# Kernel tuning notes

Measured on AMD Instinct MI355X. Metric: run time of the kernel, lower is better.

Reference implementation:

```python
import jax, jax.numpy as jnp
import numpy as np

NUM_HEADS = 16
LN_EPS = 1e-5


def setup_inputs() -> dict:
    key = jax.random.key(0)
    ks = jax.random.split(key, 5)
    B, S, H = 32768, 3, 1024
    scale = 1.0 / np.sqrt(H)
    return {
        "slots": jax.random.normal(ks[0], (B, S, H), dtype=jnp.float32),
        "in_proj_w": jax.random.normal(ks[1], (3 * H, H), dtype=jnp.float32) * scale,
        "in_proj_b": jax.random.normal(ks[2], (3 * H,), dtype=jnp.float32) * 0.02,
        "out_w": jax.random.normal(ks[3], (H, H), dtype=jnp.float32) * scale,
        "out_b": jax.random.normal(ks[4], (H,), dtype=jnp.float32) * 0.02,
        "ln_g": jnp.ones((H,), dtype=jnp.float32),
        "ln_b": jnp.zeros((H,), dtype=jnp.float32),
    }


def reference(slots, in_proj_w, in_proj_b, out_w, out_b, ln_g, ln_b):
    # slots: [B, 3, H]. Matches torch nn.MultiheadAttention (batch_first) in eval
    # mode (dropout inactive) followed by residual add + LayerNorm.
    B, S, H = slots.shape
    nh = NUM_HEADS
    dh = H // nh

    # fused QKV projection: torch does x @ in_proj_w.T + in_proj_b
    qkv = jnp.einsum("bsh,eh->bse", slots, in_proj_w) + in_proj_b  # [B,S,3H]
    q, k, v = jnp.split(qkv, 3, axis=-1)

    def heads(t):  # [B,S,H] -> [B,nh,S,dh]
        return t.reshape(B, S, nh, dh).transpose(0, 2, 1, 3)

    q, k, v = heads(q), heads(k), heads(v)

    scores = jnp.einsum("bnqd,bnkd->bnqk", q, k) / jnp.sqrt(jnp.asarray(dh, slots.dtype))
    attn = jax.nn.softmax(scores, axis=-1)  # [B,nh,3,3]
    ctx = jnp.einsum("bnqk,bnkd->bnqd", attn, v)  # [B,nh,3,dh]
    ctx = ctx.transpose(0, 2, 1, 3).reshape(B, S, H)

    attn_out = jnp.einsum("bsh,oh->bso", ctx, out_w) + out_b  # out_proj

    # residual + LayerNorm (dropout is identity at inference)
    y = slots + attn_out
    mu = jnp.mean(y, axis=-1, keepdims=True)
    var = jnp.mean(jnp.square(y - mu), axis=-1, keepdims=True)
    return (y - mu) / jnp.sqrt(var + LN_EPS) * ln_g + ln_b
```

## Files before the change

kernel.cpp:

```cpp
#include <hip/hip_runtime.h>
#include <stdint.h>

typedef unsigned short u16;
typedef float f32x4 __attribute__((ext_vector_type(4)));
typedef short bf16x8 __attribute__((ext_vector_type(8)));

__device__ __forceinline__ u16 f2bu(float f) {
  uint32_t x = __builtin_bit_cast(uint32_t, f);
  x += 0x7fffu + ((x >> 16) & 1u);
  return (u16)(x >> 16);
}
__device__ __forceinline__ float b2f(u16 u) {
  return __builtin_bit_cast(float, (uint32_t)u << 16);
}
__device__ __forceinline__ void gll16(const void* g, void* l) {
  __builtin_amdgcn_global_load_lds(
      (const __attribute__((address_space(1))) void*)g,
      (__attribute__((address_space(3))) void*)l, 16, 0, 0);
}

__global__ __launch_bounds__(256) void cvt_f32_bf16_kernel(
    const float* __restrict__ in, u16* __restrict__ out, int n4) {
  int i = blockIdx.x * 256 + threadIdx.x;
  const int stride = gridDim.x * 256;
  for (; i < n4; i += stride) {
    float4 f = reinterpret_cast<const float4*>(in)[i];
    ushort4 o;
    o.x = f2bu(f.x); o.y = f2bu(f.y); o.z = f2bu(f.z); o.w = f2bu(f.w);
    reinterpret_cast<ushort4*>(out)[i] = o;
  }
}

__global__ __launch_bounds__(512, 2) void gemm256_bt_bias(
    const u16* __restrict__ A, const u16* __restrict__ Bw,
    const float* __restrict__ bias, u16* __restrict__ C,
    int N, int K, int ntn) {
  __shared__ u16 lds[4][2][8192];
  const int tid = threadIdx.x;
  const int lane = tid & 63, wid = tid >> 6;
  const int wr = wid >> 2, wc = wid & 3;
  const int fr = lane & 15, kg = lane >> 4;

  const int cpx = (int)gridDim.x >> 3;
  const int bid = blockIdx.x;
  const int sid = (bid & 7) * cpx + (bid >> 3);
  const int mt = sid / ntn, nt = sid % ntn;

  const int srow = tid >> 2;
  const int scol = (tid & 3) ^ ((tid >> 3) & 3);
  const u16* Ag = A + (size_t)(mt * 256 + srow) * K + scol * 8;
  const u16* Bg = Bw + (size_t)(nt * 256 + srow) * K + scol * 8;
  const size_t rstep = (size_t)128 * K;

  const int sw = (fr >> 1) & 3;
  const int aoff = (wr * 128 + fr) * 32 + (kg ^ sw) * 8;
  const int boff = (wc * 64 + fr) * 32 + (kg ^ sw) * 8;

  f32x4 acc[8][4];
#pragma unroll
  for (int i = 0; i < 8; i++)
#pragma unroll
    for (int j = 0; j < 4; j++) acc[i][j] = f32x4{0.f, 0.f, 0.f, 0.f};

  const int NT = K >> 5;

#define STAGE(b, kt) do {                                   \
    const u16* a_ = Ag + (size_t)(kt) * 32;                 \
    const u16* b_ = Bg + (size_t)(kt) * 32;                 \
    gll16(a_,         &lds[(b)][0][wid * 512]);             \
    gll16(a_ + rstep, &lds[(b)][0][4096 + wid * 512]);      \
    gll16(b_,         &lds[(b)][1][wid * 512]);             \
    gll16(b_ + rstep, &lds[(b)][1][4096 + wid * 512]);      \
  } while (0)

  STAGE(0, 0);
  STAGE(1, 1);
  STAGE(2, 2);

  for (int t = 0; t < NT; t++) {
    if (t < NT - 2)       asm volatile("s_waitcnt vmcnt(8)" ::: "memory");
    else if (t == NT - 2) asm volatile("s_waitcnt vmcnt(4)" ::: "memory");
    else                  asm volatile("s_waitcnt vmcnt(0)" ::: "memory");
    __builtin_amdgcn_s_barrier();
    if (t + 3 < NT) STAGE((t + 3) & 3, t + 3);
    const u16* As = &lds[t & 3][0][0];
    const u16* Bs = &lds[t & 3][1][0];
    bf16x8 af[8], bfv[4];
#pragma unroll
    for (int mi = 0; mi < 8; mi++)
      af[mi] = *(const bf16x8*)&As[aoff + mi * 512];
#pragma unroll
    for (int nj = 0; nj < 4; nj++)
      bfv[nj] = *(const bf16x8*)&Bs[boff + nj * 512];
    __builtin_amdgcn_s_setprio(1);
#pragma unroll
    for (int mi = 0; mi < 8; mi++)
#pragma unroll
      for (int nj = 0; nj < 4; nj++)
        acc[mi][nj] = __builtin_amdgcn_mfma_f32_16x16x32_bf16(
            af[mi], bfv[nj], acc[mi][nj], 0, 0, 0);
    __builtin_amdgcn_s_setprio(0);
    asm volatile("s_waitcnt lgkmcnt(0)" ::: "memory");
    __builtin_amdgcn_sched_barrier(0);
  }
#undef STAGE

  const int crow0 = mt * 256 + wr * 128 + kg * 4;
  const int ccol0 = nt * 256 + wc * 64 + fr;
#pragma unroll
  for (int nj = 0; nj < 4; nj++) {
    const int col = ccol0 + nj * 16;
    const float bb = bias[col];
#pragma unroll
    for (int mi = 0; mi < 8; mi++) {
      const int r0 = crow0 + mi * 16;
      f32x4 v = acc[mi][nj];
#pragma unroll
      for (int r = 0; r < 4; r++)
        C[(size_t)(r0 + r) * N + col] = f2bu(v[r] + bb);
    }
  }
}

__global__ __launch_bounds__(256) void attn3_kernel(
    const u16* __restrict__ qkv, u16* __restrict__ ctx) {
  const int tid = threadIdx.x;
  const int lane = tid & 63, wid = tid >> 6;
  const int unit = blockIdx.x * 4 + wid;
  const int b = unit >> 2, hg = unit & 3;
  const size_t qbase = (size_t)b * 3 * 3072 + hg * 256 + lane * 4;

  float q[3][4], k[3][4], v[3][4];
#pragma unroll
  for (int s = 0; s < 3; s++) {
    ushort4 uq = *(const ushort4*)(qkv + qbase + (size_t)s * 3072);
    ushort4 uk = *(const ushort4*)(qkv + qbase + (size_t)s * 3072 + 1024);
    ushort4 uv = *(const ushort4*)(qkv + qbase + (size_t)s * 3072 + 2048);
    q[s][0] = b2f(uq.x); q[s][1] = b2f(uq.y); q[s][2] = b2f(uq.z); q[s][3] = b2f(uq.w);
    k[s][0] = b2f(uk.x); k[s][1] = b2f(uk.y); k[s][2] = b2f(uk.z); k[s][3] = b2f(uk.w);
    v[s][0] = b2f(uv.x); v[s][1] = b2f(uv.y); v[s][2] = b2f(uv.z); v[s][3] = b2f(uv.w);
  }

  float sc[3][3];
#pragma unroll
  for (int i = 0; i < 3; i++)
#pragma unroll
    for (int j = 0; j < 3; j++) {
      float p = q[i][0] * k[j][0] + q[i][1] * k[j][1] +
                q[i][2] * k[j][2] + q[i][3] * k[j][3];
      p += __shfl_xor(p, 1);
      p += __shfl_xor(p, 2);
      p += __shfl_xor(p, 4);
      p += __shfl_xor(p, 8);
      sc[i][j] = p;
    }

  float o[3][4];
#pragma unroll
  for (int i = 0; i < 3; i++) {
    float mx = fmaxf(sc[i][0], fmaxf(sc[i][1], sc[i][2]));
    float e0 = __expf((sc[i][0] - mx) * 0.125f);
    float e1 = __expf((sc[i][1] - mx) * 0.125f);
    float e2 = __expf((sc[i][2] - mx) * 0.125f);
    float inv = 1.f / (e0 + e1 + e2);
    e0 *= inv; e1 *= inv; e2 *= inv;
#pragma unroll
    for (int d = 0; d < 4; d++)
      o[i][d] = e0 * v[0][d] + e1 * v[1][d] + e2 * v[2][d];
  }

  const size_t obase = (size_t)b * 3 * 1024 + hg * 256 + lane * 4;
#pragma unroll
  for (int i = 0; i < 3; i++) {
    ushort4 ov;
    ov.x = f2bu(o[i][0]); ov.y = f2bu(o[i][1]);
    ov.z = f2bu(o[i][2]); ov.w = f2bu(o[i][3]);
    *(ushort4*)(ctx + obase + (size_t)i * 1024) = ov;
  }
}

__global__ __launch_bounds__(256) void ln_kernel(
    const float* __restrict__ slots, const u16* __restrict__ ao,
    const float* __restrict__ g, const float* __restrict__ bvec,
    float* __restrict__ out) {
  const int tid = threadIdx.x;
  const int lane = tid & 63, wid = tid >> 6;
  const int row = blockIdx.x * 4 + wid;
  const size_t rb = (size_t)row * 1024;

  float y[16];
  float sum = 0.f, sq = 0.f;
#pragma unroll
  for (int c = 0; c < 4; c++) {
    const int col = c * 256 + lane * 4;
    float4 sl = *(const float4*)(slots + rb + col);
    ushort4 a4 = *(const ushort4*)(ao + rb + col);
    float y0 = sl.x + b2f(a4.x), y1 = sl.y + b2f(a4.y);
    float y2 = sl.z + b2f(a4.z), y3 = sl.w + b2f(a4.w);
    y[c * 4 + 0] = y0; y[c * 4 + 1] = y1; y[c * 4 + 2] = y2; y[c * 4 + 3] = y3;
    sum += y0 + y1 + y2 + y3;
    sq += y0 * y0 + y1 * y1 + y2 * y2 + y3 * y3;
  }
#pragma unroll
  for (int m = 1; m < 64; m <<= 1) {
    sum += __shfl_xor(sum, m);
    sq  += __shfl_xor(sq, m);
  }
  const float mu = sum * (1.0f / 1024.0f);
  const float var = sq * (1.0f / 1024.0f) - mu * mu;
  const float rs = rsqrtf(var + 1e-5f);
#pragma unroll
  for (int c = 0; c < 4; c++) {
    const int col = c * 256 + lane * 4;
    float4 gg = *(const float4*)(g + col);
    float4 bb = *(const float4*)(bvec + col);
    float4 ov;
    ov.x = (y[c * 4 + 0] - mu) * rs * gg.x + bb.x;
    ov.y = (y[c * 4 + 1] - mu) * rs * gg.y + bb.y;
    ov.z = (y[c * 4 + 2] - mu) * rs * gg.z + bb.z;
    ov.w = (y[c * 4 + 3] - mu) * rs * gg.w + bb.w;
    *(float4*)(out + rb + col) = ov;
  }
}

extern "C" void kernel_launch(void* const* d_in, const int* in_sizes, int n_in,
                              void* d_out, int out_size, void* d_ws, size_t ws_size,
                              hipStream_t stream) {
  const float* slots = (const float*)d_in[0];
  const float* in_w  = (const float*)d_in[1];
  const float* in_b  = (const float*)d_in[2];
  const float* out_w = (const float*)d_in[3];
  const float* out_b = (const float*)d_in[4];
  const float* ln_g  = (const float*)d_in[5];
  const float* ln_b  = (const float*)d_in[6];
  float* out = (float*)d_out;

  const int M = 32768 * 3;

  char* ws = (char*)d_ws;
  u16* Abf   = (u16*)ws;
  u16* Winb  = (u16*)(ws + 201326592);
  u16* Woutb = (u16*)(ws + 207618048);
  u16* qkv   = (u16*)(ws + 209715200);

  cvt_f32_bf16_kernel<<<2048, 256, 0, stream>>>(slots, Abf, M * 1024 / 4);
  cvt_f32_bf16_kernel<<<2048, 256, 0, stream>>>(in_w, Winb, 3072 * 1024 / 4);
  cvt_f32_bf16_kernel<<<1024, 256, 0, stream>>>(out_w, Woutb, 1024 * 1024 / 4);

  gemm256_bt_bias<<<384 * 12, 512, 0, stream>>>(Abf, Winb, in_b, qkv, 3072, 1024, 12);

  attn3_kernel<<<32768, 256, 0, stream>>>(qkv, Abf);

  gemm256_bt_bias<<<384 * 4, 512, 0, stream>>>(Abf, Woutb, out_b, qkv, 1024, 1024, 4);

  ln_kernel<<<M / 4, 256, 0, stream>>>(slots, qkv, ln_g, ln_b, out);
}
```

Before: 1.374 ms.

## Split GEMM main loop into two half-phases interleaving LDS reads, staging, and MFMA

Restructures the bf16 GEMM K-loop into two phases per tile. Each phase loads half of the A fragments, issues half of the global-to-LDS staging (A or B) for a future tile, then runs half of the MFMAs, with barriers between phases. The goal is to overlap LDS reads and global loads with matrix math and to cut register pressure from holding all fragments at once. In exchange it adds barriers per iteration and more delicate vmcnt bookkeeping.

```diff
diff --git a/kernel.cpp b/kernel.cpp
--- a/kernel.cpp
+++ b/kernel.cpp
@@ -18,6 +18,7 @@
       (const __attribute__((address_space(1))) void*)g,
       (__attribute__((address_space(3))) void*)l, 16, 0, 0);
 }
+#define MEMFENCE asm volatile("" ::: "memory")
 
 __global__ __launch_bounds__(256) void cvt_f32_bf16_kernel(
     const float* __restrict__ in, u16* __restrict__ out, int n4) {
@@ -64,46 +65,74 @@
 
   const int NT = K >> 5;
 
-#define STAGE(b, kt) do {                                   \
+#define STAGE_A(b, kt) do {                                 \
     const u16* a_ = Ag + (size_t)(kt) * 32;                 \
-    const u16* b_ = Bg + (size_t)(kt) * 32;                 \
     gll16(a_,         &lds[(b)][0][wid * 512]);             \
     gll16(a_ + rstep, &lds[(b)][0][4096 + wid * 512]);      \
+  } while (0)
+#define STAGE_B(b, kt) do {                                 \
+    const u16* b_ = Bg + (size_t)(kt) * 32;                 \
     gll16(b_,         &lds[(b)][1][wid * 512]);             \
     gll16(b_ + rstep, &lds[(b)][1][4096 + wid * 512]);      \
   } while (0)
 
-  STAGE(0, 0);
-  STAGE(1, 1);
-  STAGE(2, 2);
+  STAGE_A(0, 0); STAGE_B(0, 0);
+  STAGE_A(1, 1); STAGE_B(1, 1);
+  STAGE_A(2, 2); STAGE_B(2, 2);
+  asm volatile("s_waitcnt vmcnt(8)" ::: "memory");
+  __builtin_amdgcn_s_barrier();
+  MEMFENCE;
 
   for (int t = 0; t < NT; t++) {
-    if (t < NT - 2)       asm volatile("s_waitcnt vmcnt(8)" ::: "memory");
-    else if (t == NT - 2) asm volatile("s_waitcnt vmcnt(4)" ::: "memory");
-    else                  asm volatile("s_waitcnt vmcnt(0)" ::: "memory");
-    __builtin_amdgcn_s_barrier();
-    if (t + 3 < NT) STAGE((t + 3) & 3, t + 3);
     const u16* As = &lds[t & 3][0][0];
     const u16* Bs = &lds[t & 3][1][0];
-    bf16x8 af[8], bfv[4];
-#pragma unroll
-    for (int mi = 0; mi < 8; mi++)
+
+    bf16x8 bv[4], af[4];
+#pragma unroll
+    for (int nj = 0; nj < 4; nj++)
+      bv[nj] = *(const bf16x8*)&Bs[boff + nj * 512];
+#pragma unroll
+    for (int mi = 0; mi < 4; mi++)
       af[mi] = *(const bf16x8*)&As[aoff + mi * 512];
-#pragma unroll
-    for (int nj = 0; nj < 4; nj++)
-      bfv[nj] = *(const bf16x8*)&Bs[boff + nj * 512];
+    if (t + 3 < NT) STAGE_A((t + 3) & 3, t + 3);
+    __builtin_amdgcn_s_barrier();
+    MEMFENCE;
     __builtin_amdgcn_s_setprio(1);
 #pragma unroll
-    for (int mi = 0; mi < 8; mi++)
+    for (int mi = 0; mi < 4; mi++)
 #pragma unroll
       for (int nj = 0; nj < 4; nj++)
         acc[mi][nj] = __builtin_amdgcn_mfma_f32_16x16x32_bf16(
-            af[mi], bfv[nj], acc[mi][nj], 0, 0, 0);
+            af[mi], bv[nj], acc[mi][nj], 0, 0, 0);
     __builtin_amdgcn_s_setprio(0);
-    asm volatile("s_waitcnt lgkmcnt(0)" ::: "memory");
-    __builtin_amdgcn_sched_barrier(0);
-  }
-#undef STAGE
+    __builtin_amdgcn_s_barrier();
+    MEMFENCE;
+
+    bf16x8 ag[4];
+#pragma unroll
+    for (int mi = 0; mi < 4; mi++)
+      ag[mi] = *(const bf16x8*)&As[aoff + 2048 + mi * 512];
+    if (t + 3 < NT) STAGE_B((t + 3) & 3, t + 3);
+    if (t <= NT - 4)      asm volatile("s_waitcnt vmcnt(8)" ::: "memory");
+    else if (t == NT - 3) asm volatile("s_waitcnt vmcnt(4)" ::: "memory");
+    else if (t == NT - 2) asm volatile("s_waitcnt vmcnt(0)" ::: "memory");
+    __builtin_amdgcn_s_barrier();
+    MEMFENCE;
+    __builtin_amdgcn_s_setprio(1);
+#pragma unroll
+    for (int mi = 0; mi < 4; mi++)
+#pragma unroll
+      for (int nj = 0; nj < 4; nj++)
+        acc[4 + mi][nj] = __builtin_amdgcn_mfma_f32_16x16x32_bf16(
+            ag[mi], bv[nj], acc[4 + mi][nj], 0, 0, 0);
+    __builtin_amdgcn_s_setprio(0);
+    if (t < NT - 1) {
+      __builtin_amdgcn_s_barrier();
+      MEMFENCE;
+    }
+  }
+#undef STAGE_A
+#undef STAGE_B
 
   const int crow0 = mt * 256 + wr * 128 + kg * 4;
   const int ccol0 = nt * 256 + wc * 64 + fr;
```

New measurement: 1.397 ms. No clear change (+1.7%).

## Restructure GEMM main loop into double-buffered, barrier-interleaved half-tile schedule

Applied to the files above, without the earlier changes.

Replaces the 4-deep ring of 32-wide K stages with a 2-buffer scheme over 64-wide K tiles split into halves. Each tile's MFMA work is divided into four phases separated by barriers, and each phase issues the next tile's A or B global-to-LDS load. The aim is to interleave memory traffic with compute more finely, in the style of ping-pong schedules, while keeping LDS usage the same. The cost is many more barriers per iteration and a shallower prefetch depth, which may expose load latency.

```diff
diff --git a/kernel.cpp b/kernel.cpp
--- a/kernel.cpp
+++ b/kernel.cpp
@@ -18,6 +18,8 @@
       (const __attribute__((address_space(1))) void*)g,
       (__attribute__((address_space(3))) void*)l, 16, 0, 0);
 }
+#define MEMFENCE asm volatile("" ::: "memory")
+#define BAR() do { __builtin_amdgcn_s_barrier(); MEMFENCE; } while (0)
 
 __global__ __launch_bounds__(256) void cvt_f32_bf16_kernel(
     const float* __restrict__ in, u16* __restrict__ out, int n4) {
@@ -35,7 +37,7 @@
     const u16* __restrict__ A, const u16* __restrict__ Bw,
     const float* __restrict__ bias, u16* __restrict__ C,
     int N, int K, int ntn) {
-  __shared__ u16 lds[4][2][8192];
+  __shared__ u16 lds[2][2][2][8192];
   const int tid = threadIdx.x;
   const int lane = tid & 63, wid = tid >> 6;
   const int wr = wid >> 2, wc = wid & 3;
@@ -53,8 +55,9 @@
   const size_t rstep = (size_t)128 * K;
 
   const int sw = (fr >> 1) & 3;
-  const int aoff = (wr * 128 + fr) * 32 + (kg ^ sw) * 8;
-  const int boff = (wc * 64 + fr) * 32 + (kg ^ sw) * 8;
+  const int kgs = (kg ^ sw) * 8;
+  const int aoff = (wr * 128 + fr) * 32 + kgs;
+  const int boff = (wc * 64 + fr) * 32 + kgs;
 
   f32x4 acc[8][4];
 #pragma unroll
@@ -62,48 +65,97 @@
 #pragma unroll
     for (int j = 0; j < 4; j++) acc[i][j] = f32x4{0.f, 0.f, 0.f, 0.f};
 
-  const int NT = K >> 5;
-
-#define STAGE(b, kt) do {                                   \
-    const u16* a_ = Ag + (size_t)(kt) * 32;                 \
-    const u16* b_ = Bg + (size_t)(kt) * 32;                 \
-    gll16(a_,         &lds[(b)][0][wid * 512]);             \
-    gll16(a_ + rstep, &lds[(b)][0][4096 + wid * 512]);      \
-    gll16(b_,         &lds[(b)][1][wid * 512]);             \
-    gll16(b_ + rstep, &lds[(b)][1][4096 + wid * 512]);      \
+  const int NT = K >> 6;
+
+#define STAGE_A(kh, kt, nb) do {                               \
+    const u16* s_ = Ag + (size_t)(kt) * 64 + (kh) * 32;        \
+    gll16(s_,         &lds[nb][0][kh][wid * 512]);             \
+    gll16(s_ + rstep, &lds[nb][0][kh][4096 + wid * 512]);      \
   } while (0)
-
-  STAGE(0, 0);
-  STAGE(1, 1);
-  STAGE(2, 2);
+#define STAGE_B(kh, kt, nb) do {                               \
+    const u16* s_ = Bg + (size_t)(kt) * 64 + (kh) * 32;        \
+    gll16(s_,         &lds[nb][1][kh][wid * 512]);             \
+    gll16(s_ + rstep, &lds[nb][1][kh][4096 + wid * 512]);      \
+  } while (0)
+
+  STAGE_A(0, 0, 0); STAGE_B(0, 0, 0);
+  STAGE_A(1, 0, 0); STAGE_B(1, 0, 0);
+  asm volatile("s_waitcnt vmcnt(4)" ::: "memory");
+  BAR();
 
   for (int t = 0; t < NT; t++) {
-    if (t < NT - 2)       asm volatile("s_waitcnt vmcnt(8)" ::: "memory");
-    else if (t == NT - 2) asm volatile("s_waitcnt vmcnt(4)" ::: "memory");
-    else                  asm volatile("s_waitcnt vmcnt(0)" ::: "memory");
-    __builtin_amdgcn_s_barrier();
-    if (t + 3 < NT) STAGE((t + 3) & 3, t + 3);
-    const u16* As = &lds[t & 3][0][0];
-    const u16* Bs = &lds[t & 3][1][0];
-    bf16x8 af[8], bfv[4];
+    const int buf = t & 1, nb = buf ^ 1;
+    const bool st = (t + 1 < NT);
+    const u16* As0 = &lds[buf][0][0][0];
+    const u16* As1 = &lds[buf][0][1][0];
+    const u16* Bs0 = &lds[buf][1][0][0];
+    const u16* Bs1 = &lds[buf][1][1][0];
+
+    bf16x8 av[8], bv[2];
+
 #pragma unroll
     for (int mi = 0; mi < 8; mi++)
-      af[mi] = *(const bf16x8*)&As[aoff + mi * 512];
-#pragma unroll
-    for (int nj = 0; nj < 4; nj++)
-      bfv[nj] = *(const bf16x8*)&Bs[boff + nj * 512];
+      av[mi] = *(const bf16x8*)&As0[aoff + mi * 512];
+    bv[0] = *(const bf16x8*)&Bs0[boff];
+    bv[1] = *(const bf16x8*)&Bs0[boff + 512];
+    if (st) STAGE_A(0, t + 1, nb);
+    BAR();
     __builtin_amdgcn_s_setprio(1);
 #pragma unroll
+    for (int mi = 0; mi < 8; mi++) {
+      acc[mi][0] = __builtin_amdgcn_mfma_f32_16x16x32_bf16(av[mi], bv[0], acc[mi][0], 0, 0, 0);
+      acc[mi][1] = __builtin_amdgcn_mfma_f32_16x16x32_bf16(av[mi], bv[1], acc[mi][1], 0, 0, 0);
+    }
+    __builtin_amdgcn_s_setprio(0);
+    BAR();
+
+    bv[0] = *(const bf16x8*)&Bs0[boff + 1024];
+    bv[1] = *(const bf16x8*)&Bs0[boff + 1536];
+    if (st) STAGE_B(0, t + 1, nb);
+    BAR();
+    __builtin_amdgcn_s_setprio(1);
+#pragma unroll
+    for (int mi = 0; mi < 8; mi++) {
+      acc[mi][2] = __builtin_amdgcn_mfma_f32_16x16x32_bf16(av[mi], bv[0], acc[mi][2], 0, 0, 0);
+      acc[mi][3] = __builtin_amdgcn_mfma_f32_16x16x32_bf16(av[mi], bv[1], acc[mi][3], 0, 0, 0);
+    }
+    __builtin_amdgcn_s_setprio(0);
+    if (t == NT - 1) asm volatile("s_waitcnt vmcnt(0)" ::: "memory");
+    else             asm volatile("s_waitcnt vmcnt(4)" ::: "memory");
+    BAR();
+
+#pragma unroll
     for (int mi = 0; mi < 8; mi++)
-#pragma unroll
-      for (int nj = 0; nj < 4; nj++)
-        acc[mi][nj] = __builtin_amdgcn_mfma_f32_16x16x32_bf16(
-            af[mi], bfv[nj], acc[mi][nj], 0, 0, 0);
+      av[mi] = *(const bf16x8*)&As1[aoff + mi * 512];
+    bv[0] = *(const bf16x8*)&Bs1[boff];
+    bv[1] = *(const bf16x8*)&Bs1[boff + 512];
+    if (st) STAGE_A(1, t + 1, nb);
+    BAR();
+    __builtin_amdgcn_s_setprio(1);
+#pragma unroll
+    for (int mi = 0; mi < 8; mi++) {
+      acc[mi][0] = __builtin_amdgcn_mfma_f32_16x16x32_bf16(av[mi], bv[0], acc[mi][0], 0, 0, 0);
+      acc[mi][1] = __builtin_amdgcn_mfma_f32_16x16x32_bf16(av[mi], bv[1], acc[mi][1], 0, 0, 0);
+    }
     __builtin_amdgcn_s_setprio(0);
-    asm volatile("s_waitcnt lgkmcnt(0)" ::: "memory");
-    __builtin_amdgcn_sched_barrier(0);
-  }
-#undef STAGE
+    BAR();
+
+    bv[0] = *(const bf16x8*)&Bs1[boff + 1024];
+    bv[1] = *(const bf16x8*)&Bs1[boff + 1536];
+    if (st) STAGE_B(1, t + 1, nb);
+    BAR();
+    __builtin_amdgcn_s_setprio(1);
+#pragma unroll
+    for (int mi = 0; mi < 8; mi++) {
+      acc[mi][2] = __builtin_amdgcn_mfma_f32_16x16x32_bf16(av[mi], bv[0], acc[mi][2], 0, 0, 0);
+      acc[mi][3] = __builtin_amdgcn_mfma_f32_16x16x32_bf16(av[mi], bv[1], acc[mi][3], 0, 0, 0);
+    }
+    __builtin_amdgcn_s_setprio(0);
+    asm volatile("s_waitcnt vmcnt(4)" ::: "memory");
+    BAR();
+  }
+#undef STAGE_A
+#undef STAGE_B
 
   const int crow0 = mt * 256 + wr * 128 + kg * 4;
   const int ccol0 = nt * 256 + wc * 64 + fr;
```

New measurement: 1.360 ms. Within noise of the previous version (-1.0%).

## Switch GEMM to double-buffered LDS with syncthreads and grid-stride attention

Applied to the files above, without the earlier changes.

Cuts the GEMM LDS ring from four stages to two and replaces the explicit vmcnt-counted prefetch-three-ahead scheme with a simple prefetch-one-ahead plus __syncthreads. This halves LDS use (64KB to 32KB), which may allow more resident blocks, but it shortens the global-load lookahead and puts a full barrier in every iteration. The attention kernel also becomes a grid-stride loop launched with 2048 blocks instead of 32768, to reduce block launch overhead.

```diff
diff --git a/kernel.cpp b/kernel.cpp
--- a/kernel.cpp
+++ b/kernel.cpp
@@ -35,7 +35,7 @@
     const u16* __restrict__ A, const u16* __restrict__ Bw,
     const float* __restrict__ bias, u16* __restrict__ C,
     int N, int K, int ntn) {
-  __shared__ u16 lds[4][2][8192];
+  __shared__ u16 lds[2][2][8192];
   const int tid = threadIdx.x;
   const int lane = tid & 63, wid = tid >> 6;
   const int wr = wid >> 2, wc = wid & 3;
@@ -53,8 +53,9 @@
   const size_t rstep = (size_t)128 * K;
 
   const int sw = (fr >> 1) & 3;
-  const int aoff = (wr * 128 + fr) * 32 + (kg ^ sw) * 8;
-  const int boff = (wc * 64 + fr) * 32 + (kg ^ sw) * 8;
+  const int kgs = (kg ^ sw) * 8;
+  const int aoff = (wr * 128 + fr) * 32 + kgs;
+  const int boff = (wc * 64 + fr) * 32 + kgs;
 
   f32x4 acc[8][4];
 #pragma unroll
@@ -74,34 +75,29 @@
   } while (0)
 
   STAGE(0, 0);
-  STAGE(1, 1);
-  STAGE(2, 2);
+  __syncthreads();
 
   for (int t = 0; t < NT; t++) {
-    if (t < NT - 2)       asm volatile("s_waitcnt vmcnt(8)" ::: "memory");
-    else if (t == NT - 2) asm volatile("s_waitcnt vmcnt(4)" ::: "memory");
-    else                  asm volatile("s_waitcnt vmcnt(0)" ::: "memory");
-    __builtin_amdgcn_s_barrier();
-    if (t + 3 < NT) STAGE((t + 3) & 3, t + 3);
-    const u16* As = &lds[t & 3][0][0];
-    const u16* Bs = &lds[t & 3][1][0];
-    bf16x8 af[8], bfv[4];
+    const int cur = t & 1;
+    if (t + 1 < NT) STAGE(cur ^ 1, t + 1);
+    const u16* As = &lds[cur][0][0];
+    const u16* Bs = &lds[cur][1][0];
+    bf16x8 a[8], b[4];
 #pragma unroll
     for (int mi = 0; mi < 8; mi++)
-      af[mi] = *(const bf16x8*)&As[aoff + mi * 512];
+      a[mi] = *(const bf16x8*)&As[aoff + mi * 512];
 #pragma unroll
     for (int nj = 0; nj < 4; nj++)
-      bfv[nj] = *(const bf16x8*)&Bs[boff + nj * 512];
+      b[nj] = *(const bf16x8*)&Bs[boff + nj * 512];
     __builtin_amdgcn_s_setprio(1);
 #pragma unroll
     for (int mi = 0; mi < 8; mi++)
 #pragma unroll
       for (int nj = 0; nj < 4; nj++)
         acc[mi][nj] = __builtin_amdgcn_mfma_f32_16x16x32_bf16(
-            af[mi], bfv[nj], acc[mi][nj], 0, 0, 0);
+            a[mi], b[nj], acc[mi][nj], 0, 0, 0);
     __builtin_amdgcn_s_setprio(0);
-    asm volatile("s_waitcnt lgkmcnt(0)" ::: "memory");
-    __builtin_amdgcn_sched_barrier(0);
+    __syncthreads();
   }
 #undef STAGE
 
@@ -126,56 +122,58 @@
     const u16* __restrict__ qkv, u16* __restrict__ ctx) {
   const int tid = threadIdx.x;
   const int lane = tid & 63, wid = tid >> 6;
-  const int unit = blockIdx.x * 4 + wid;
-  const int b = unit >> 2, hg = unit & 3;
-  const size_t qbase = (size_t)b * 3 * 3072 + hg * 256 + lane * 4;
-
-  float q[3][4], k[3][4], v[3][4];
-#pragma unroll
-  for (int s = 0; s < 3; s++) {
-    ushort4 uq = *(const ushort4*)(qkv + qbase + (size_t)s * 3072);
-    ushort4 uk = *(const ushort4*)(qkv + qbase + (size_t)s * 3072 + 1024);
-    ushort4 uv = *(const ushort4*)(qkv + qbase + (size_t)s * 3072 + 2048);
-    q[s][0] = b2f(uq.x); q[s][1] = b2f(uq.y); q[s][2] = b2f(uq.z); q[s][3] = b2f(uq.w);
-    k[s][0] = b2f(uk.x); k[s][1] = b2f(uk.y); k[s][2] = b2f(uk.z); k[s][3] = b2f(uk.w);
-    v[s][0] = b2f(uv.x); v[s][1] = b2f(uv.y); v[s][2] = b2f(uv.z); v[s][3] = b2f(uv.w);
-  }
-
-  float sc[3][3];
-#pragma unroll
-  for (int i = 0; i < 3; i++)
-#pragma unroll
-    for (int j = 0; j < 3; j++) {
-      float p = q[i][0] * k[j][0] + q[i][1] * k[j][1] +
-                q[i][2] * k[j][2] + q[i][3] * k[j][3];
-      p += __shfl_xor(p, 1);
-      p += __shfl_xor(p, 2);
-      p += __shfl_xor(p, 4);
-      p += __shfl_xor(p, 8);
-      sc[i][j] = p;
-    }
-
-  float o[3][4];
-#pragma unroll
-  for (int i = 0; i < 3; i++) {
-    float mx = fmaxf(sc[i][0], fmaxf(sc[i][1], sc[i][2]));
-    float e0 = __expf((sc[i][0] - mx) * 0.125f);
-    float e1 = __expf((sc[i][1] - mx) * 0.125f);
-    float e2 = __expf((sc[i][2] - mx) * 0.125f);
-    float inv = 1.f / (e0 + e1 + e2);
-    e0 *= inv; e1 *= inv; e2 *= inv;
-#pragma unroll
-    for (int d = 0; d < 4; d++)
-      o[i][d] = e0 * v[0][d] + e1 * v[1][d] + e2 * v[2][d];
-  }
-
-  const size_t obase = (size_t)b * 3 * 1024 + hg * 256 + lane * 4;
-#pragma unroll
-  for (int i = 0; i < 3; i++) {
-    ushort4 ov;
-    ov.x = f2bu(o[i][0]); ov.y = f2bu(o[i][1]);
-    ov.z = f2bu(o[i][2]); ov.w = f2bu(o[i][3]);
-    *(ushort4*)(ctx + obase + (size_t)i * 1024) = ov;
+  const int nunit = 32768 * 4;
+  for (int unit = blockIdx.x * 4 + wid; unit < nunit; unit += gridDim.x * 4) {
+    const int b = unit >> 2, hg = unit & 3;
+    const size_t qbase = (size_t)b * 3 * 3072 + hg * 256 + lane * 4;
+
+    float q[3][4], k[3][4], v[3][4];
+#pragma unroll
+    for (int s = 0; s < 3; s++) {
+      ushort4 uq = *(const ushort4*)(qkv + qbase + (size_t)s * 3072);
+      ushort4 uk = *(const ushort4*)(qkv + qbase + (size_t)s * 3072 + 1024);
+      ushort4 uv = *(const ushort4*)(qkv + qbase + (size_t)s * 3072 + 2048);
+      q[s][0] = b2f(uq.x); q[s][1] = b2f(uq.y); q[s][2] = b2f(uq.z); q[s][3] = b2f(uq.w);
+      k[s][0] = b2f(uk.x); k[s][1] = b2f(uk.y); k[s][2] = b2f(uk.z); k[s][3] = b2f(uk.w);
+      v[s][0] = b2f(uv.x); v[s][1] = b2f(uv.y); v[s][2] = b2f(uv.z); v[s][3] = b2f(uv.w);
+    }
+
+    float sc[3][3];
+#pragma unroll
+    for (int i = 0; i < 3; i++)
+#pragma unroll
+      for (int j = 0; j < 3; j++) {
+        float p = q[i][0] * k[j][0] + q[i][1] * k[j][1] +
+                  q[i][2] * k[j][2] + q[i][3] * k[j][3];
+        p += __shfl_xor(p, 1);
+        p += __shfl_xor(p, 2);
+        p += __shfl_xor(p, 4);
+        p += __shfl_xor(p, 8);
+        sc[i][j] = p;
+      }
+
+    float o[3][4];
+#pragma unroll
+    for (int i = 0; i < 3; i++) {
+      float mx = fmaxf(sc[i][0], fmaxf(sc[i][1], sc[i][2]));
+      float e0 = __expf((sc[i][0] - mx) * 0.125f);
+      float e1 = __expf((sc[i][1] - mx) * 0.125f);
+      float e2 = __expf((sc[i][2] - mx) * 0.125f);
+      float inv = 1.f / (e0 + e1 + e2);
+      e0 *= inv; e1 *= inv; e2 *= inv;
+#pragma unroll
+      for (int d = 0; d < 4; d++)
+        o[i][d] = e0 * v[0][d] + e1 * v[1][d] + e2 * v[2][d];
+    }
+
+    const size_t obase = (size_t)b * 3 * 1024 + hg * 256 + lane * 4;
+#pragma unroll
+    for (int i = 0; i < 3; i++) {
+      ushort4 ov;
+      ov.x = f2bu(o[i][0]); ov.y = f2bu(o[i][1]);
+      ov.z = f2bu(o[i][2]); ov.w = f2bu(o[i][3]);
+      *(ushort4*)(ctx + obase + (size_t)i * 1024) = ov;
+    }
   }
 }
 
@@ -249,7 +247,7 @@
 
   gemm256_bt_bias<<<384 * 12, 512, 0, stream>>>(Abf, Winb, in_b, qkv, 3072, 1024, 12);
 
-  attn3_kernel<<<32768, 256, 0, stream>>>(qkv, Abf);
+  attn3_kernel<<<2048, 256, 0, stream>>>(qkv, Abf);
 
   gemm256_bt_bias<<<384 * 4, 512, 0, stream>>>(Abf, Woutb, out_b, qkv, 1024, 1024, 4);
 
```

Result: slower. 1.429 ms (+4.0%).
